# Performance work log

Measured on AMD Instinct MI355X. Metric: run time of the kernel, lower is better.

The kernel has to match this reference:

```python
import jax, jax.numpy as jnp
import numpy as np

B, S, E, H, BS = 4, 4096, 1024, 1024, 128  # batch, seq, embed, head_size, block_size


def setup_inputs() -> dict:
    key = jax.random.key(0)
    k1, k2, k3, k4 = jax.random.split(key, 4)
    x = jax.random.normal(k1, (B, S, E), dtype=jnp.float32)
    W_qkv = jax.random.normal(k2, (E, 3 * H), dtype=jnp.float32) * (E ** -0.5)
    W_out = jax.random.normal(k3, (H, H), dtype=jnp.float32) * (H ** -0.5)
    b_out = jax.random.normal(k4, (H,), dtype=jnp.float32) * 0.01
    return {"x": x, "W_qkv": W_qkv, "W_out": W_out, "b_out": b_out}


def reference(x, W_qkv, W_out, b_out):
    b, s, e = x.shape
    h = W_out.shape[1]
    nb = s // BS  # number of blocks (block-diagonal attention)
    qkv = x @ W_qkv                      # [B, S, 3H]
    q, k, v = jnp.split(qkv, 3, axis=-1)

    def blk(t):
        return t.reshape(b, nb, BS, h)   # [B, nb, BS, H]

    scale = h ** -0.5
    # each query block attends only its own key/value block
    scores = jnp.einsum('bnqd,bnkd->bnqk', blk(q), blk(k)) * scale  # [B, nb, BS, BS]
    causal = jnp.tril(jnp.ones((BS, BS), dtype=bool))  # diagonal block of full tril
    scores = jnp.where(causal, scores, -jnp.inf)
    scores = scores - jnp.max(scores, axis=-1, keepdims=True)
    p = jnp.exp(scores)
    p = p / (jnp.sum(p, axis=-1, keepdims=True) + 1e-6)  # faithful: softmax with +1e-6 eps
    out = jnp.einsum('bnqk,bnkd->bnqd', p, blk(v)).reshape(b, s, h)
    return out @ W_out.T + b_out
```

## Files before the change

### kernel.cpp

```cpp
#include <hip/hip_runtime.h>
#include <hip/hip_bf16.h>

typedef __attribute__((ext_vector_type(8))) short short8;
typedef __attribute__((ext_vector_type(4))) float float4_;

typedef const __attribute__((address_space(1))) void* gas_t;
typedef __attribute__((address_space(3))) void* las_t;

__device__ __forceinline__ void gl_lds16(const void* g, void* l) {
  __builtin_amdgcn_global_load_lds((gas_t)g, (las_t)l, 16, 0, 0);
}

__device__ __forceinline__ short f2b(float f) {
  union { __hip_bfloat16 h; short s; } u;
  u.h = __float2bfloat16(f);
  return u.s;
}
__device__ __forceinline__ short8 cvt8(float4_ lo, float4_ hi) {
  short8 r;
#pragma unroll
  for (int t = 0; t < 4; t++) { r[t] = f2b(lo[t]); r[t + 4] = f2b(hi[t]); }
  return r;
}

__global__ __launch_bounds__(256) void prep(
    const float* __restrict__ Wqkv, short* __restrict__ WqkvT,
    const float* __restrict__ Wout, short* __restrict__ Woutb,
    const float* __restrict__ x, short* __restrict__ xb, int has_x)
{
  __shared__ __align__(16) short T[64 * 72];
  const int b   = blockIdx.x;
  const int tid = threadIdx.x;
  if (b < 768) {
    const int R = 1024, C = 3072;
    const int r0 = (b / 48) * 64;
    const int c0 = (b % 48) * 64;
    const int r  = tid >> 2;
    const int cp = (tid & 3) * 16;
#pragma unroll
    for (int g = 0; g < 4; g++) {
      float4_ v = *(const float4_*)&Wqkv[(long)(r0 + r) * C + c0 + cp + g * 4];
#pragma unroll
      for (int t = 0; t < 4; t++) T[(cp + g * 4 + t) * 72 + r] = f2b(v[t]);
    }
    __syncthreads();
    const int c  = tid >> 2;
    const int rp = (tid & 3) * 16;
    short8 w0 = *(const short8*)&T[c * 72 + rp];
    short8 w1 = *(const short8*)&T[c * 72 + rp + 8];
    *(short8*)&WqkvT[(long)(c0 + c) * R + r0 + rp] = w0;
    *(short8*)&WqkvT[(long)(c0 + c) * R + r0 + rp + 8] = w1;
  } else if (b < 1280) {
    const long i = ((long)(b - 768) * 256 + tid) * 8;
    float4_ lo = *(const float4_*)&Wout[i];
    float4_ hi = *(const float4_*)&Wout[i + 4];
    *(short8*)&Woutb[i] = cvt8(lo, hi);
  } else if (has_x) {
    const long i = ((long)(b - 1280) * 256 + tid) * 8;
    float4_ lo = *(const float4_*)&x[i];
    float4_ hi = *(const float4_*)&x[i + 4];
    *(short8*)&xb[i] = cvt8(lo, hi);
  }
}

__global__ __launch_bounds__(256) void gemm_bt(
    const void* __restrict__ Av, int lda, int a_f32,
    const short* __restrict__ B,
    void* __restrict__ Cv, int ldc, int c_f32,
    int K, const float* __restrict__ bias)
{
  __shared__ __align__(16) short As[128 * 64];
  __shared__ __align__(16) short Bs[128 * 64];
  const int tid  = threadIdx.x;
  const int lane = tid & 63;
  const int w    = tid >> 6;
  const int quad = lane >> 4;
  const int l15  = lane & 15;
  const int wm   = (w >> 1) * 64;
  const int wn   = (w & 1) * 64;

  const int nx  = gridDim.x;
  const int nwg = nx * gridDim.y;
  int wid = blockIdx.y * nx + blockIdx.x;
  if ((nwg & 7) == 0) wid = (wid & 7) * (nwg >> 3) + (wid >> 3);
  const int m0 = (wid / nx) * 128;
  const int n0 = (wid % nx) * 128;

  float4_ acc[4][4] = {};

  const int srow = tid >> 3;
  const int sk   = tid & 7;
  const int kswz = ((sk ^ (srow & 7)) * 8);
  const int wbase = w * 512;
  const int frow = tid >> 1;
  const int fh   = tid & 1;

  for (int k0 = 0; k0 < K; k0 += 64) {
    short8 fs[4];
    if (a_f32) {
      const float* Af = (const float*)Av;
#pragma unroll
      for (int g = 0; g < 2; g++) {
        float4_ v0 = *(const float4_*)&Af[(long)(m0 + frow) * lda + k0 + fh * 32 + g * 16];
        float4_ v1 = *(const float4_*)&Af[(long)(m0 + frow) * lda + k0 + fh * 32 + g * 16 + 4];
        float4_ v2 = *(const float4_*)&Af[(long)(m0 + frow) * lda + k0 + fh * 32 + g * 16 + 8];
        float4_ v3 = *(const float4_*)&Af[(long)(m0 + frow) * lda + k0 + fh * 32 + g * 16 + 12];
        fs[g * 2]     = cvt8(v0, v1);
        fs[g * 2 + 1] = cvt8(v2, v3);
      }
    }
    __syncthreads();
    if (a_f32) {
#pragma unroll
      for (int g = 0; g < 4; g++) {
        const int c_log = fh * 4 + g;
        *(short8*)&As[frow * 64 + ((c_log ^ (frow & 7)) * 8)] = fs[g];
      }
    } else {
      const short* Ab = (const short*)Av;
#pragma unroll
      for (int g = 0; g < 4; g++)
        gl_lds16(&Ab[(long)(m0 + g * 32 + srow) * lda + k0 + kswz],
                 &As[g * 2048 + wbase]);
    }
#pragma unroll
    for (int g = 0; g < 4; g++)
      gl_lds16(&B[(long)(n0 + g * 32 + srow) * K + k0 + kswz],
               &Bs[g * 2048 + wbase]);
    __syncthreads();
#pragma unroll
    for (int kk = 0; kk < 2; kk++) {
      short8 a[4], b[4];
#pragma unroll
      for (int i = 0; i < 4; i++)
        a[i] = *(const short8*)&As[(wm + i * 16 + l15) * 64 + ((kk * 4 + quad) ^ (l15 & 7)) * 8];
#pragma unroll
      for (int j = 0; j < 4; j++)
        b[j] = *(const short8*)&Bs[(wn + j * 16 + l15) * 64 + ((kk * 4 + quad) ^ (l15 & 7)) * 8];
#pragma unroll
      for (int i = 0; i < 4; i++)
#pragma unroll
        for (int j = 0; j < 4; j++)
          acc[i][j] = __builtin_amdgcn_mfma_f32_16x16x32_bf16(a[i], b[j], acc[i][j], 0, 0, 0);
    }
  }

  const int gidx = w >> 1;
  for (int i = 0; i < 4; i++) {
    __syncthreads();
    if (c_f32) {
      float* scr = (float*)As;
#pragma unroll
      for (int j = 0; j < 4; j++) {
        const int col = wn + j * 16 + l15;
        const float bv = bias ? bias[n0 + col] : 0.0f;
#pragma unroll
        for (int r = 0; r < 4; r++) {
          const int row = gidx * 16 + quad * 4 + r;
          scr[row * 128 + (col ^ ((row & 7) << 4))] = acc[i][j][r] + bv;
        }
      }
    } else {
#pragma unroll
      for (int j = 0; j < 4; j++) {
        const int col = wn + j * 16 + l15;
#pragma unroll
        for (int r = 0; r < 4; r++) {
          const int row = gidx * 16 + quad * 4 + r;
          As[row * 128 + (col ^ ((row & 7) << 4))] = f2b(acc[i][j][r]);
        }
      }
    }
    __syncthreads();
    const int rs   = tid >> 3;
    const int colp = (tid & 7) * 16;
    const int cs   = colp ^ ((rs & 7) << 4);
    const long row_g = m0 + (rs >> 4) * 64 + i * 16 + (rs & 15);
    if (c_f32) {
      float* C = (float*)Cv;
      const float* scr = (const float*)As;
#pragma unroll
      for (int q = 0; q < 4; q++) {
        float4_ v = *(const float4_*)&scr[rs * 128 + cs + q * 4];
        *(float4_*)&C[row_g * ldc + n0 + colp + q * 4] = v;
      }
    } else {
      short* C = (short*)Cv;
      short8 v0 = *(const short8*)&As[rs * 128 + cs];
      short8 v1 = *(const short8*)&As[rs * 128 + cs + 8];
      *(short8*)&C[row_g * ldc + n0 + colp]     = v0;
      *(short8*)&C[row_g * ldc + n0 + colp + 8] = v1;
    }
  }
}

template<int NJ>
__device__ __forceinline__ void attn_body(short* __restrict__ qkv, int tile,
                                          short* smem)
{
  constexpr int NK    = NJ * 16;
  constexpr int QROW0 = (NJ == 8) ? 64 : 0;
  constexpr int KCALLS = NK / 32;

  short* Ps = smem;
  short* U  = smem + 8704;

  const int tid  = threadIdx.x;
  const int t8   = tid & 255;
  const int g    = tid >> 8;
  const int wl   = (tid >> 6) & 3;
  const int lane = tid & 63;
  const int quad = lane >> 4;
  const int l15  = lane & 15;
  const long base = (long)tile * 128 * 3072;

  const short* Qg = qkv + base + (long)QROW0 * 3072;
  const short* Kg = qkv + base + 1024;
  const short* Vg = qkv + base + 2048;

  short* Qs = U + g * 4096;
  short* Ks = U + 8192 + g * 8192;
  const int srow8 = t8 >> 3;
  const int sk    = t8 & 7;
  const int kswz  = (sk ^ (srow8 & 7)) * 8;
  const int wb    = wl * 512;

  float4_ acc[NJ] = {};

  for (int i = 0; i < 8; i++) {
    const int k0 = g * 64 + i * 128;
    __syncthreads();
#pragma unroll
    for (int c = 0; c < 2; c++)
      gl_lds16(&Qg[(long)(c * 32 + srow8) * 3072 + k0 + kswz], &Qs[c * 2048 + wb]);
#pragma unroll
    for (int c = 0; c < KCALLS; c++)
      gl_lds16(&Kg[(long)(c * 32 + srow8) * 3072 + k0 + kswz], &Ks[c * 2048 + wb]);
    __syncthreads();
#pragma unroll
    for (int kk = 0; kk < 2; kk++) {
      const int ch = ((kk * 4 + quad) ^ (l15 & 7)) * 8;
      short8 a = *(const short8*)&Qs[(wl * 16 + l15) * 64 + ch];
#pragma unroll
      for (int j = 0; j < NJ; j++) {
        short8 b = *(const short8*)&Ks[(j * 16 + l15) * 64 + ch];
        acc[j] = __builtin_amdgcn_mfma_f32_16x16x32_bf16(a, b, acc[j], 0, 0, 0);
      }
    }
  }
  __syncthreads();

  float* Sscr = (float*)U;
  if (g == 1) {
#pragma unroll
    for (int r = 0; r < 4; r++) {
      const int rowq = wl * 16 + quad * 4 + r;
#pragma unroll
      for (int j = 0; j < NJ; j++)
        Sscr[rowq * 132 + j * 16 + l15] = acc[j][r];
    }
  }
  __syncthreads();
  if (g == 0) {
    const float scale = 0.03125f;
#pragma unroll
    for (int r = 0; r < 4; r++) {
      const int rowq = wl * 16 + quad * 4 + r;
      float s[NJ];
      float mx = -3.0e38f;
#pragma unroll
      for (int j = 0; j < NJ; j++) {
        const int col = j * 16 + l15;
        const float v = (acc[j][r] + Sscr[rowq * 132 + col]) * scale;
        s[j] = (col <= QROW0 + rowq) ? v : -3.0e38f;
        mx = fmaxf(mx, s[j]);
      }
      mx = fmaxf(mx, __shfl_xor(mx, 1));
      mx = fmaxf(mx, __shfl_xor(mx, 2));
      mx = fmaxf(mx, __shfl_xor(mx, 4));
      mx = fmaxf(mx, __shfl_xor(mx, 8));
      float p[NJ];
      float sum = 0.0f;
#pragma unroll
      for (int j = 0; j < NJ; j++) {
        p[j] = (s[j] > -1.0e38f) ? __expf(s[j] - mx) : 0.0f;
        sum += p[j];
      }
      sum += __shfl_xor(sum, 1);
      sum += __shfl_xor(sum, 2);
      sum += __shfl_xor(sum, 4);
      sum += __shfl_xor(sum, 8);
      const float inv = 1.0f / (sum + 1e-6f);
#pragma unroll
      for (int j = 0; j < NJ; j++)
        Ps[rowq * 136 + j * 16 + l15] = f2b(p[j] * inv);
    }
  }
  __syncthreads();

  short* Vt = U + g * 8704;
  short* Ot = U + 17408 + g * 4608;
  short* Op = qkv + base + (long)QROW0 * 3072;

  for (int i = 0; i < 8; i++) {
    const int d0 = g * 64 + i * 128;
    __syncthreads();
    if (NJ == 8) {
      const int kr = t8 >> 1, dp = (t8 & 1) * 32;
#pragma unroll
      for (int gg = 0; gg < 4; gg++) {
        short8 v = *(const short8*)&Vg[(long)kr * 3072 + d0 + dp + gg * 8];
#pragma unroll
        for (int t = 0; t < 8; t++) Vt[(dp + gg * 8 + t) * 136 + kr] = v[t];
      }
    } else {
      const int kr = t8 >> 2, dp = (t8 & 3) * 16;
#pragma unroll
      for (int gg = 0; gg < 2; gg++) {
        short8 v = *(const short8*)&Vg[(long)kr * 3072 + d0 + dp + gg * 8];
#pragma unroll
        for (int t = 0; t < 8; t++) Vt[(dp + gg * 8 + t) * 136 + kr] = v[t];
      }
    }
    __syncthreads();
    float4_ o[4] = {};
#pragma unroll
    for (int kk = 0; kk < NK / 32; kk++) {
      short8 a = *(const short8*)&Ps[(wl * 16 + l15) * 136 + kk * 32 + quad * 8];
#pragma unroll
      for (int j = 0; j < 4; j++) {
        short8 b = *(const short8*)&Vt[(j * 16 + l15) * 136 + kk * 32 + quad * 8];
        o[j] = __builtin_amdgcn_mfma_f32_16x16x32_bf16(a, b, o[j], 0, 0, 0);
      }
    }
#pragma unroll
    for (int j = 0; j < 4; j++)
#pragma unroll
      for (int r = 0; r < 4; r++)
        Ot[(wl * 16 + quad * 4 + r) * 72 + j * 16 + l15] = f2b(o[j][r]);
    __syncthreads();
    const int orow = t8 >> 2, ocp = (t8 & 3) * 16;
    short8 v0 = *(const short8*)&Ot[orow * 72 + ocp];
    short8 v1 = *(const short8*)&Ot[orow * 72 + ocp + 8];
    *(short8*)&Op[(long)orow * 3072 + d0 + ocp]     = v0;
    *(short8*)&Op[(long)orow * 3072 + d0 + ocp + 8] = v1;
  }
}

__global__ __launch_bounds__(512) void attn_blockdiag(short* __restrict__ qkv)
{
  __shared__ __align__(16) short smem[35328];
  const int tile = blockIdx.x >> 1;
  if (blockIdx.x & 1) attn_body<8>(qkv, tile, smem);
  else                attn_body<4>(qkv, tile, smem);
}

extern "C" void kernel_launch(void* const* d_in, const int* in_sizes, int n_in,
                              void* d_out, int out_size, void* d_ws, size_t ws_size,
                              hipStream_t stream) {
  const float* x    = (const float*)d_in[0];
  const float* Wqkv = (const float*)d_in[1];
  const float* Wout = (const float*)d_in[2];
  const float* bout = (const float*)d_in[3];
  float* out = (float*)d_out;

  char* ws = (char*)d_ws;
  short* WqkvT = (short*)ws;
  short* Woutb = (short*)(ws + 6291456);
  short* qkv   = (short*)(ws + 8388608);
  short* xb    = (short*)(ws + 8388608 + (size_t)16384 * 3072 * 2);

  if (ws_size >= 8388608 + (size_t)16384 * 3072 * 2 + (size_t)16384 * 1024 * 2) {
    prep<<<9472, 256, 0, stream>>>(Wqkv, WqkvT, Wout, Woutb, x, xb, 1);
    gemm_bt<<<dim3(24, 128), 256, 0, stream>>>(xb, 1024, 0, WqkvT,
                                               qkv, 3072, 0, 1024, nullptr);
    attn_blockdiag<<<dim3(256), 512, 0, stream>>>(qkv);
    gemm_bt<<<dim3(8, 128), 256, 0, stream>>>(qkv, 3072, 0, Woutb,
                                              out, 1024, 1, 1024, bout);
  } else if (ws_size >= 8388608 + (size_t)16384 * 3072 * 2) {
    prep<<<1280, 256, 0, stream>>>(Wqkv, WqkvT, Wout, Woutb, nullptr, nullptr, 0);
    gemm_bt<<<dim3(24, 128), 256, 0, stream>>>(x, 1024, 1, WqkvT,
                                               qkv, 3072, 0, 1024, nullptr);
    attn_blockdiag<<<dim3(256), 512, 0, stream>>>(qkv);
    gemm_bt<<<dim3(8, 128), 256, 0, stream>>>(qkv, 3072, 0, Woutb,
                                              out, 1024, 1, 1024, bout);
  } else {
    prep<<<1280, 256, 0, stream>>>(Wqkv, WqkvT, Wout, Woutb, nullptr, nullptr, 0);
    for (int c = 0; c < 4; c++) {
      const float* xc = x + (long)c * 4096 * 1024;
      float* outc = out + (long)c * 4096 * 1024;
      gemm_bt<<<dim3(24, 32), 256, 0, stream>>>(xc, 1024, 1, WqkvT,
                                                qkv, 3072, 0, 1024, nullptr);
      attn_blockdiag<<<dim3(64), 512, 0, stream>>>(qkv);
      gemm_bt<<<dim3(8, 32), 256, 0, stream>>>(qkv, 3072, 0, Woutb,
                                               outc, 1024, 1, 1024, bout);
    }
  }
}
```

Baseline: 328.5 us.

## Add 256x128 triple-buffered 8-wave GEMM kernel with interleaved async LDS loads

Measured after the change: 449.0 us. 1.37x slower.

```diff
diff --git a/kernel.cpp b/kernel.cpp
--- a/kernel.cpp
+++ b/kernel.cpp
@@ -22,6 +22,10 @@
   for (int t = 0; t < 4; t++) { r[t] = f2b(lo[t]); r[t + 4] = f2b(hi[t]); }
   return r;
 }
+
+#define SBAR() do { __builtin_amdgcn_sched_barrier(0); \
+                    __builtin_amdgcn_s_barrier(); \
+                    __builtin_amdgcn_sched_barrier(0); } while (0)
 
 __global__ __launch_bounds__(256) void prep(
     const float* __restrict__ Wqkv, short* __restrict__ WqkvT,
@@ -63,6 +67,189 @@
   }
 }
 
+__global__ __launch_bounds__(512, 2) void g256(
+    const short* __restrict__ A, int lda,
+    const short* __restrict__ B,
+    void* __restrict__ Cv, int ldc, int c_f32,
+    int K, const float* __restrict__ bias)
+{
+  __shared__ __align__(16) short smem[3 * 24576];
+  const int tid  = threadIdx.x;
+  const int w    = tid >> 6;
+  const int lane = tid & 63;
+  const int quad = lane >> 4;
+  const int l15  = lane & 15;
+  const int wr   = w >> 1;
+  const int wc   = w & 1;
+  const int sr   = tid >> 3;
+  const int sc   = tid & 7;
+  const int kswz = (sc ^ (sr & 7)) * 8;
+  const int wbase = w * 512;
+
+  const int nx  = gridDim.x;
+  const int nwg = nx * gridDim.y;
+  int wid = blockIdx.y * nx + blockIdx.x;
+  if ((nwg & 7) == 0) wid = (wid & 7) * (nwg >> 3) + (wid >> 3);
+  const int m0 = (wid / nx) * 256;
+  const int n0 = (wid % nx) * 128;
+
+  const int nkt = K >> 6;
+
+#pragma unroll
+  for (int tt = 0; tt < 2; ++tt) {
+    short* Ax = &smem[tt * 24576];
+    short* Bx = Ax + 16384;
+#pragma unroll
+    for (int c = 0; c < 4; ++c)
+      gl_lds16(&A[(long)(m0 + c * 64 + sr) * lda + tt * 64 + kswz],
+               &Ax[c * 4096 + wbase]);
+#pragma unroll
+    for (int c = 0; c < 2; ++c)
+      gl_lds16(&B[(long)(n0 + c * 64 + sr) * K + tt * 64 + kswz],
+               &Bx[c * 4096 + wbase]);
+  }
+  asm volatile("s_waitcnt vmcnt(6)" ::: "memory");
+  SBAR();
+
+  float4_ acc[4][4] = {};
+  int bt = 0;
+
+#pragma unroll 1
+  for (int t = 0; t < nkt; ++t) {
+    const short* At = &smem[bt * 24576];
+    const short* Bt = At + 16384;
+    short* Ai = &smem[((bt >= 1) ? (bt - 1) : 2) * 24576];
+    short* Bi = Ai + 16384;
+    const int  ti    = t + 2;
+    const bool issue = ti < nkt;
+    const long tk    = (long)ti * 64;
+    short8 a[4];
+
+    {
+      const int ch = (quad ^ (l15 & 7)) * 8;
+#pragma unroll
+      for (int mi = 0; mi < 4; ++mi)
+        a[mi] = *(const short8*)&At[(wr * 64 + mi * 16 + l15) * 64 + ch];
+      short8 b0 = *(const short8*)&Bt[(wc * 64 + l15) * 64 + ch];
+      short8 b1 = *(const short8*)&Bt[(wc * 64 + 16 + l15) * 64 + ch];
+      if (issue) {
+        gl_lds16(&A[(long)(m0 + sr) * lda + tk + kswz],      &Ai[wbase]);
+        gl_lds16(&A[(long)(m0 + 64 + sr) * lda + tk + kswz], &Ai[4096 + wbase]);
+      }
+      SBAR();
+      __builtin_amdgcn_s_setprio(1);
+#pragma unroll
+      for (int mi = 0; mi < 4; ++mi) {
+        acc[mi][0] = __builtin_amdgcn_mfma_f32_16x16x32_bf16(a[mi], b0, acc[mi][0], 0, 0, 0);
+        acc[mi][1] = __builtin_amdgcn_mfma_f32_16x16x32_bf16(a[mi], b1, acc[mi][1], 0, 0, 0);
+      }
+      __builtin_amdgcn_s_setprio(0);
+      SBAR();
+    }
+    {
+      const int ch = (quad ^ (l15 & 7)) * 8;
+      short8 b0 = *(const short8*)&Bt[(wc * 64 + 32 + l15) * 64 + ch];
+      short8 b1 = *(const short8*)&Bt[(wc * 64 + 48 + l15) * 64 + ch];
+      if (issue) {
+        gl_lds16(&A[(long)(m0 + 128 + sr) * lda + tk + kswz], &Ai[8192 + wbase]);
+        gl_lds16(&A[(long)(m0 + 192 + sr) * lda + tk + kswz], &Ai[12288 + wbase]);
+      }
+      SBAR();
+      __builtin_amdgcn_s_setprio(1);
+#pragma unroll
+      for (int mi = 0; mi < 4; ++mi) {
+        acc[mi][2] = __builtin_amdgcn_mfma_f32_16x16x32_bf16(a[mi], b0, acc[mi][2], 0, 0, 0);
+        acc[mi][3] = __builtin_amdgcn_mfma_f32_16x16x32_bf16(a[mi], b1, acc[mi][3], 0, 0, 0);
+      }
+      __builtin_amdgcn_s_setprio(0);
+      SBAR();
+    }
+    {
+      const int ch = ((4 + quad) ^ (l15 & 7)) * 8;
+#pragma unroll
+      for (int mi = 0; mi < 4; ++mi)
+        a[mi] = *(const short8*)&At[(wr * 64 + mi * 16 + l15) * 64 + ch];
+      short8 b0 = *(const short8*)&Bt[(wc * 64 + l15) * 64 + ch];
+      short8 b1 = *(const short8*)&Bt[(wc * 64 + 16 + l15) * 64 + ch];
+      if (issue)
+        gl_lds16(&B[(long)(n0 + sr) * K + tk + kswz], &Bi[wbase]);
+      SBAR();
+      __builtin_amdgcn_s_setprio(1);
+#pragma unroll
+      for (int mi = 0; mi < 4; ++mi) {
+        acc[mi][0] = __builtin_amdgcn_mfma_f32_16x16x32_bf16(a[mi], b0, acc[mi][0], 0, 0, 0);
+        acc[mi][1] = __builtin_amdgcn_mfma_f32_16x16x32_bf16(a[mi], b1, acc[mi][1], 0, 0, 0);
+      }
+      __builtin_amdgcn_s_setprio(0);
+      SBAR();
+    }
+    {
+      const int ch = ((4 + quad) ^ (l15 & 7)) * 8;
+      short8 b0 = *(const short8*)&Bt[(wc * 64 + 32 + l15) * 64 + ch];
+      short8 b1 = *(const short8*)&Bt[(wc * 64 + 48 + l15) * 64 + ch];
+      if (issue)
+        gl_lds16(&B[(long)(n0 + 64 + sr) * K + tk + kswz], &Bi[4096 + wbase]);
+      if (issue)            { asm volatile("s_waitcnt vmcnt(6)" ::: "memory"); }
+      else if (ti == nkt)   { asm volatile("s_waitcnt vmcnt(0)" ::: "memory"); }
+      SBAR();
+      __builtin_amdgcn_s_setprio(1);
+#pragma unroll
+      for (int mi = 0; mi < 4; ++mi) {
+        acc[mi][2] = __builtin_amdgcn_mfma_f32_16x16x32_bf16(a[mi], b0, acc[mi][2], 0, 0, 0);
+        acc[mi][3] = __builtin_amdgcn_mfma_f32_16x16x32_bf16(a[mi], b1, acc[mi][3], 0, 0, 0);
+      }
+      __builtin_amdgcn_s_setprio(0);
+      SBAR();
+    }
+    bt = (bt == 2) ? 0 : bt + 1;
+  }
+
+  float* scrf = (float*)smem;
+  short* scrh = (short*)smem;
+#pragma unroll 1
+  for (int i = 0; i < 4; ++i) {
+    __syncthreads();
+    if (c_f32) {
+#pragma unroll
+      for (int ni = 0; ni < 4; ++ni) {
+        const int col = wc * 64 + ni * 16 + l15;
+        const float bv = bias ? bias[n0 + col] : 0.0f;
+#pragma unroll
+        for (int r = 0; r < 4; ++r) {
+          const int row = wr * 16 + quad * 4 + r;
+          scrf[row * 128 + (col ^ ((row & 7) << 4))] = acc[i][ni][r] + bv;
+        }
+      }
+    } else {
+#pragma unroll
+      for (int ni = 0; ni < 4; ++ni) {
+        const int col = wc * 64 + ni * 16 + l15;
+#pragma unroll
+        for (int r = 0; r < 4; ++r) {
+          const int row = wr * 16 + quad * 4 + r;
+          scrh[row * 128 + (col ^ ((row & 7) << 4))] = f2b(acc[i][ni][r]);
+        }
+      }
+    }
+    __syncthreads();
+    const int rs   = tid >> 3;
+    const int colp = (tid & 7) * 16;
+    const int cs   = colp ^ ((rs & 7) << 4);
+    const long row_g = m0 + (rs >> 4) * 64 + i * 16 + (rs & 15);
+    if (c_f32) {
+      float* C = (float*)Cv;
+#pragma unroll
+      for (int q = 0; q < 4; ++q)
+        *(float4_*)&C[row_g * ldc + n0 + colp + q * 4] =
+            *(const float4_*)&scrf[rs * 128 + cs + q * 4];
+    } else {
+      short* C = (short*)Cv;
+      *(short8*)&C[row_g * ldc + n0 + colp]     = *(const short8*)&scrh[rs * 128 + cs];
+      *(short8*)&C[row_g * ldc + n0 + colp + 8] = *(const short8*)&scrh[rs * 128 + cs + 8];
+    }
+  }
+}
+
 __global__ __launch_bounds__(256) void gemm_bt(
     const void* __restrict__ Av, int lda, int a_f32,
     const short* __restrict__ B,
@@ -372,18 +559,18 @@
 
   if (ws_size >= 8388608 + (size_t)16384 * 3072 * 2 + (size_t)16384 * 1024 * 2) {
     prep<<<9472, 256, 0, stream>>>(Wqkv, WqkvT, Wout, Woutb, x, xb, 1);
-    gemm_bt<<<dim3(24, 128), 256, 0, stream>>>(xb, 1024, 0, WqkvT,
-                                               qkv, 3072, 0, 1024, nullptr);
+    g256<<<dim3(24, 64), 512, 0, stream>>>(xb, 1024, WqkvT,
+                                           qkv, 3072, 0, 1024, nullptr);
     attn_blockdiag<<<dim3(256), 512, 0, stream>>>(qkv);
-    gemm_bt<<<dim3(8, 128), 256, 0, stream>>>(qkv, 3072, 0, Woutb,
-                                              out, 1024, 1, 1024, bout);
+    g256<<<dim3(8, 64), 512, 0, stream>>>(qkv, 3072, Woutb,
+                                          out, 1024, 1, 1024, bout);
   } else if (ws_size >= 8388608 + (size_t)16384 * 3072 * 2) {
     prep<<<1280, 256, 0, stream>>>(Wqkv, WqkvT, Wout, Woutb, nullptr, nullptr, 0);
     gemm_bt<<<dim3(24, 128), 256, 0, stream>>>(x, 1024, 1, WqkvT,
                                                qkv, 3072, 0, 1024, nullptr);
     attn_blockdiag<<<dim3(256), 512, 0, stream>>>(qkv);
-    gemm_bt<<<dim3(8, 128), 256, 0, stream>>>(qkv, 3072, 0, Woutb,
-                                              out, 1024, 1, 1024, bout);
+    g256<<<dim3(8, 64), 512, 0, stream>>>(qkv, 3072, Woutb,
+                                          out, 1024, 1, 1024, bout);
   } else {
     prep<<<1280, 256, 0, stream>>>(Wqkv, WqkvT, Wout, Woutb, nullptr, nullptr, 0);
     for (int c = 0; c < 4; c++) {
@@ -392,8 +579,8 @@
       gemm_bt<<<dim3(24, 32), 256, 0, stream>>>(xc, 1024, 1, WqkvT,
                                                 qkv, 3072, 0, 1024, nullptr);
       attn_blockdiag<<<dim3(64), 512, 0, stream>>>(qkv);
-      gemm_bt<<<dim3(8, 32), 256, 0, stream>>>(qkv, 3072, 0, Woutb,
-                                               outc, 1024, 1, 1024, bout);
-    }
-  }
-}
+      g256<<<dim3(8, 16), 512, 0, stream>>>(qkv, 3072, Woutb,
+                                            outc, 1024, 1, 1024, bout);
+    }
+  }
+}
```
